# Performance work log

Hardware: AMD Instinct MI355X
Metric: run time of the kernel (lower is better)

The kernel has to match this reference:

```python
import jax, jax.numpy as jnp
import numpy as np

NUM_PROCS = 16
PROC_DIM = 8
SPATIAL_DIM = 3
NUM_LOCS = 500000
NAUG = NUM_PROCS * NUM_LOCS  # 8M augmented rows


def setup_inputs() -> dict:
    key = jax.random.key(0)
    k1, k2, k3, k4 = jax.random.split(key, 4)
    proc_pos = jax.random.normal(k1, (NUM_PROCS, PROC_DIM), dtype=jnp.float32)
    locs_sp = jax.random.normal(k2, (NUM_LOCS, SPATIAL_DIM), dtype=jnp.float32)
    process_ids = jax.random.randint(k3, (NAUG,), 0, NUM_PROCS, dtype=jnp.int64)
    location_ids = jax.random.randint(k4, (NAUG,), 0, NUM_LOCS, dtype=jnp.int64)
    return {
        "proc_pos": proc_pos,
        "locs_sp": locs_sp,
        "process_ids": process_ids,
        "location_ids": location_ids,
    }


def reference(proc_pos, locs_sp, process_ids, location_ids):
    # Fused gather-concat: equivalent to the per-row loop of
    # concat([proc_pos[pid], locs_sp[lid]]) stacked over all augmented rows.
    # [NAUG, PROC_DIM] and [NAUG, SPATIAL_DIM] gathers, then concat on feature axis.
    proc_part = jnp.take(proc_pos, process_ids, axis=0)
    loc_part = jnp.take(locs_sp, location_ids, axis=0)
    locs_augmented = jnp.concatenate([proc_part, loc_part], axis=1)  # [NAUG, PROC_DIM+SPATIAL_DIM]
    return locs_augmented
```

## Files before the change

### kernel.cpp

```cpp
#include <hip/hip_runtime.h>

#define NUM_PROCS 16
#define PROC_DIM 8
#define SPATIAL_DIM 3
#define ROW_DIM (PROC_DIM + SPATIAL_DIM)
#define BLOCK 256
#define WAVES_PB (BLOCK / 64)
#define RPT 2
#define TROWS (64 * RPT)
#define TILE_F (TROWS * ROW_DIM)
#define SPROC_STRIDE 12

typedef float v4f __attribute__((ext_vector_type(4)));
typedef int   v2i __attribute__((ext_vector_type(2)));

__global__ __launch_bounds__(BLOCK) void gather_concat_kernel(
    const float* __restrict__ proc_pos,
    const float* __restrict__ locs_sp,
    const int*   __restrict__ process_ids,
    const int*   __restrict__ location_ids,
    float* __restrict__ out,
    int naug)
{
    __shared__ float sproc[NUM_PROCS * SPROC_STRIDE];
    __shared__ float stage[WAVES_PB][TILE_F];

    const int t    = threadIdx.x;
    const int wv   = t >> 6;
    const int lane = t & 63;

    if (t < NUM_PROCS * PROC_DIM)
        sproc[(t >> 3) * SPROC_STRIDE + (t & 7)] = proc_pos[t];
    __syncthreads();

    const int WT = naug / TROWS;
    const int gw = blockIdx.x * WAVES_PB + wv;
    const int NW = gridDim.x * WAVES_PB;

    float* const sl      = stage[wv];
    const v4f* const s4  = (const v4f*)sl;

    v2i pidC = {0, 0}, lidC = {0, 0};
    v2i pidN = {0, 0}, lidN = {0, 0};
    float ca0=0, ca1=0, ca2=0, cb0=0, cb1=0, cb2=0;

    const int wt0 = gw;
    const int wt1 = gw + NW;
    if (wt0 < WT) {
        pidC = __builtin_nontemporal_load((const v2i*)(process_ids + (size_t)wt0 * TROWS) + lane);
        lidC = __builtin_nontemporal_load((const v2i*)(location_ids + (size_t)wt0 * TROWS) + lane);
    }
    if (wt1 < WT) {
        pidN = __builtin_nontemporal_load((const v2i*)(process_ids + (size_t)wt1 * TROWS) + lane);
        lidN = __builtin_nontemporal_load((const v2i*)(location_ids + (size_t)wt1 * TROWS) + lane);
    }
    if (wt0 < WT) {
        const float* l0 = locs_sp + (size_t)lidC.x * SPATIAL_DIM;
        const float* l1 = locs_sp + (size_t)lidC.y * SPATIAL_DIM;
        ca0 = l0[0]; ca1 = l0[1]; ca2 = l0[2];
        cb0 = l1[0]; cb1 = l1[1]; cb2 = l1[2];
    }

    for (int wt = wt0; wt < WT; wt += NW) {
        const int wtn  = wt + NW;
        const int wtnn = wt + 2 * NW;

        v2i pidT = {0, 0}, lidT = {0, 0};
        if (wtnn < WT) {
            pidT = __builtin_nontemporal_load((const v2i*)(process_ids + (size_t)wtnn * TROWS) + lane);
            lidT = __builtin_nontemporal_load((const v2i*)(location_ids + (size_t)wtnn * TROWS) + lane);
        }

        float na0=0, na1=0, na2=0, nb0=0, nb1=0, nb2=0;
        if (wtn < WT) {
            const float* l0 = locs_sp + (size_t)lidN.x * SPATIAL_DIM;
            const float* l1 = locs_sp + (size_t)lidN.y * SPATIAL_DIM;
            na0 = l0[0]; na1 = l0[1]; na2 = l0[2];
            nb0 = l1[0]; nb1 = l1[1]; nb2 = l1[2];
        }

        const v4f* P0 = (const v4f*)(sproc + pidC.x * SPROC_STRIDE);
        const v4f* P1 = (const v4f*)(sproc + pidC.y * SPROC_STRIDE);
        v4f p00 = P0[0], p01 = P0[1];
        v4f p10 = P1[0], p11 = P1[1];
        float* d0 = sl + (size_t)(2 * lane) * ROW_DIM;
        d0[0] = p00.x; d0[1] = p00.y; d0[2]  = p00.z; d0[3] = p00.w;
        d0[4] = p01.x; d0[5] = p01.y; d0[6]  = p01.z; d0[7] = p01.w;
        d0[8] = ca0;   d0[9] = ca1;   d0[10] = ca2;
        float* d1 = d0 + ROW_DIM;
        d1[0] = p10.x; d1[1] = p10.y; d1[2]  = p10.z; d1[3] = p10.w;
        d1[4] = p11.x; d1[5] = p11.y; d1[6]  = p11.z; d1[7] = p11.w;
        d1[8] = cb0;   d1[9] = cb1;   d1[10] = cb2;

        v4f* out4 = (v4f*)(out + (size_t)wt * TILE_F);
        #pragma unroll
        for (int k = 0; k < 5; ++k) {
            const int i = lane + k * 64;
            __builtin_nontemporal_store(s4[i], out4 + i);
        }
        if (lane < 32) {
            const int i = 320 + lane;
            __builtin_nontemporal_store(s4[i], out4 + i);
        }

        pidC = pidN; lidC = lidN; pidN = pidT; lidN = lidT;
        ca0 = na0; ca1 = na1; ca2 = na2;
        cb0 = nb0; cb1 = nb1; cb2 = nb2;
    }

    const int tail0 = WT * TROWS;
    if (gw == 0) {
        for (int r = tail0 + lane; r < naug; r += 64) {
            const int pid = process_ids[r];
            const int lid = location_ids[r];
            const float* ps = sproc + pid * SPROC_STRIDE;
            const float* ls = locs_sp + (size_t)lid * SPATIAL_DIM;
            float* orow = out + (size_t)r * ROW_DIM;
            #pragma unroll
            for (int j = 0; j < PROC_DIM; ++j) orow[j] = ps[j];
            orow[8] = ls[0]; orow[9] = ls[1]; orow[10] = ls[2];
        }
    }
}

extern "C" void kernel_launch(void* const* d_in, const int* in_sizes, int n_in,
                              void* d_out, int out_size, void* d_ws, size_t ws_size,
                              hipStream_t stream) {
    const float* proc_pos     = (const float*)d_in[0];
    const float* locs_sp      = (const float*)d_in[1];
    const int*   process_ids  = (const int*)d_in[2];
    const int*   location_ids = (const int*)d_in[3];
    float* out = (float*)d_out;

    const int naug = in_sizes[2];
    const int WT   = naug / TROWS;

    int grid = 1792;
    if (grid * WAVES_PB > WT) grid = (WT + WAVES_PB - 1) / WAVES_PB;
    if (grid < 1) grid = 1;

    gather_concat_kernel<<<grid, BLOCK, 0, stream>>>(
        proc_pos, locs_sp, process_ids, location_ids, out, naug);
}
```

Before: 461.2 us.

## Deepen gather prefetch pipeline with one row per lane and larger grid

Each lane now handles one row per tile instead of two, with 64-row tiles. The software pipeline is deepened to keep location-id loads five tiles ahead and location gathers three tiles ahead, so more random gathers are in flight per wave. The change also sets a launch-bounds occupancy hint of 8 and raises the grid from 1792 to 2048 blocks. The aim is to hide gather latency better, at the cost of more registers per lane and more loop iterations with smaller stores.

```diff
diff --git a/kernel.cpp b/kernel.cpp
--- a/kernel.cpp
+++ b/kernel.cpp
@@ -6,15 +6,13 @@
 #define ROW_DIM (PROC_DIM + SPATIAL_DIM)
 #define BLOCK 256
 #define WAVES_PB (BLOCK / 64)
-#define RPT 2
-#define TROWS (64 * RPT)
+#define TROWS 64
 #define TILE_F (TROWS * ROW_DIM)
 #define SPROC_STRIDE 12
 
 typedef float v4f __attribute__((ext_vector_type(4)));
-typedef int   v2i __attribute__((ext_vector_type(2)));
 
-__global__ __launch_bounds__(BLOCK) void gather_concat_kernel(
+__global__ __launch_bounds__(BLOCK, 8) void gather_concat_kernel(
     const float* __restrict__ proc_pos,
     const float* __restrict__ locs_sp,
     const int*   __restrict__ process_ids,
@@ -34,78 +32,64 @@
     __syncthreads();
 
     const int WT = naug / TROWS;
+    const int NW = gridDim.x * WAVES_PB;
     const int gw = blockIdx.x * WAVES_PB + wv;
-    const int NW = gridDim.x * WAVES_PB;
 
-    float* const sl      = stage[wv];
-    const v4f* const s4  = (const v4f*)sl;
+    float* const sl     = stage[wv];
+    const v4f* const s4 = (const v4f*)sl;
 
-    v2i pidC = {0, 0}, lidC = {0, 0};
-    v2i pidN = {0, 0}, lidN = {0, 0};
-    float ca0=0, ca1=0, ca2=0, cb0=0, cb1=0, cb2=0;
+    auto ld_lid = [&](int w) -> int {
+        return (w < WT) ? __builtin_nontemporal_load(location_ids + (size_t)w * TROWS + lane) : 0;
+    };
+    auto ld_pid = [&](int w) -> int {
+        return (w < WT) ? __builtin_nontemporal_load(process_ids + (size_t)w * TROWS + lane) : 0;
+    };
 
-    const int wt0 = gw;
-    const int wt1 = gw + NW;
-    if (wt0 < WT) {
-        pidC = __builtin_nontemporal_load((const v2i*)(process_ids + (size_t)wt0 * TROWS) + lane);
-        lidC = __builtin_nontemporal_load((const v2i*)(location_ids + (size_t)wt0 * TROWS) + lane);
-    }
-    if (wt1 < WT) {
-        pidN = __builtin_nontemporal_load((const v2i*)(process_ids + (size_t)wt1 * TROWS) + lane);
-        lidN = __builtin_nontemporal_load((const v2i*)(location_ids + (size_t)wt1 * TROWS) + lane);
-    }
-    if (wt0 < WT) {
-        const float* l0 = locs_sp + (size_t)lidC.x * SPATIAL_DIM;
-        const float* l1 = locs_sp + (size_t)lidC.y * SPATIAL_DIM;
-        ca0 = l0[0]; ca1 = l0[1]; ca2 = l0[2];
-        cb0 = l1[0]; cb1 = l1[1]; cb2 = l1[2];
-    }
+    int li0  = ld_lid(gw);
+    int li1  = ld_lid(gw + NW);
+    int li2  = ld_lid(gw + 2 * NW);
+    int liA  = ld_lid(gw + 3 * NW);
+    int liB  = ld_lid(gw + 4 * NW);
+    int pidA = ld_pid(gw);
+    int pidB = ld_pid(gw + NW);
 
-    for (int wt = wt0; wt < WT; wt += NW) {
-        const int wtn  = wt + NW;
-        const int wtnn = wt + 2 * NW;
+    const float* g0 = locs_sp + (size_t)li0 * SPATIAL_DIM;
+    const float* g1 = locs_sp + (size_t)li1 * SPATIAL_DIM;
+    const float* g2 = locs_sp + (size_t)li2 * SPATIAL_DIM;
+    float c0  = g0[0], c1  = g0[1], c2  = g0[2];
+    float n10 = g1[0], n11 = g1[1], n12 = g1[2];
+    float n20 = g2[0], n21 = g2[1], n22 = g2[2];
 
-        v2i pidT = {0, 0}, lidT = {0, 0};
-        if (wtnn < WT) {
-            pidT = __builtin_nontemporal_load((const v2i*)(process_ids + (size_t)wtnn * TROWS) + lane);
-            lidT = __builtin_nontemporal_load((const v2i*)(location_ids + (size_t)wtnn * TROWS) + lane);
-        }
+    for (int wt = gw; wt < WT; wt += NW) {
+        int liC   = ld_lid(wt + 5 * NW);
+        int pidC_ = ld_pid(wt + 2 * NW);
 
-        float na0=0, na1=0, na2=0, nb0=0, nb1=0, nb2=0;
-        if (wtn < WT) {
-            const float* l0 = locs_sp + (size_t)lidN.x * SPATIAL_DIM;
-            const float* l1 = locs_sp + (size_t)lidN.y * SPATIAL_DIM;
-            na0 = l0[0]; na1 = l0[1]; na2 = l0[2];
-            nb0 = l1[0]; nb1 = l1[1]; nb2 = l1[2];
-        }
+        const float* g3 = locs_sp + (size_t)liA * SPATIAL_DIM;
+        float n30 = g3[0], n31 = g3[1], n32 = g3[2];
 
-        const v4f* P0 = (const v4f*)(sproc + pidC.x * SPROC_STRIDE);
-        const v4f* P1 = (const v4f*)(sproc + pidC.y * SPROC_STRIDE);
-        v4f p00 = P0[0], p01 = P0[1];
-        v4f p10 = P1[0], p11 = P1[1];
-        float* d0 = sl + (size_t)(2 * lane) * ROW_DIM;
-        d0[0] = p00.x; d0[1] = p00.y; d0[2]  = p00.z; d0[3] = p00.w;
-        d0[4] = p01.x; d0[5] = p01.y; d0[6]  = p01.z; d0[7] = p01.w;
-        d0[8] = ca0;   d0[9] = ca1;   d0[10] = ca2;
-        float* d1 = d0 + ROW_DIM;
-        d1[0] = p10.x; d1[1] = p10.y; d1[2]  = p10.z; d1[3] = p10.w;
-        d1[4] = p11.x; d1[5] = p11.y; d1[6]  = p11.z; d1[7] = p11.w;
-        d1[8] = cb0;   d1[9] = cb1;   d1[10] = cb2;
+        const v4f* P = (const v4f*)(sproc + pidA * SPROC_STRIDE);
+        v4f pa = P[0], pb = P[1];
+        float* d = sl + lane * ROW_DIM;
+        d[0] = pa.x; d[1] = pa.y; d[2]  = pa.z; d[3] = pa.w;
+        d[4] = pb.x; d[5] = pb.y; d[6]  = pb.z; d[7] = pb.w;
+        d[8] = c0;   d[9] = c1;   d[10] = c2;
 
         v4f* out4 = (v4f*)(out + (size_t)wt * TILE_F);
-        #pragma unroll
-        for (int k = 0; k < 5; ++k) {
+        #pragma unroll 1
+        for (int k = 0; k < 2; ++k) {
             const int i = lane + k * 64;
             __builtin_nontemporal_store(s4[i], out4 + i);
         }
-        if (lane < 32) {
-            const int i = 320 + lane;
+        if (lane < 48) {
+            const int i = 128 + lane;
             __builtin_nontemporal_store(s4[i], out4 + i);
         }
 
-        pidC = pidN; lidC = lidN; pidN = pidT; lidN = lidT;
-        ca0 = na0; ca1 = na1; ca2 = na2;
-        cb0 = nb0; cb1 = nb1; cb2 = nb2;
+        c0  = n10; c1  = n11; c2  = n12;
+        n10 = n20; n11 = n21; n12 = n22;
+        n20 = n30; n21 = n31; n22 = n32;
+        liA = liB; liB = liC;
+        pidA = pidB; pidB = pidC_;
     }
 
     const int tail0 = WT * TROWS;
@@ -135,8 +119,9 @@
     const int naug = in_sizes[2];
     const int WT   = naug / TROWS;
 
-    int grid = 1792;
-    if (grid * WAVES_PB > WT) grid = (WT + WAVES_PB - 1) / WAVES_PB;
+    int grid = 2048;
+    const int maxg = (WT + WAVES_PB - 1) / WAVES_PB;
+    if (maxg >= 1 && grid > maxg) grid = maxg;
     if (grid < 1) grid = 1;
 
     gather_concat_kernel<<<grid, BLOCK, 0, stream>>>(
```

After: 470.5 us. 1.02x slower.
